# Performance work log

Measured on AMD Instinct MI355X. Metric: run time of the kernel, lower is better.

The kernel has to match this reference:

```python
import jax, jax.numpy as jnp
import numpy as np

H = 128; L = 4; N_TOTAL = 2500; M = 4; K = 12
S = N_TOTAL * M          # 10000 subgraphs
F = S * K                # 120000 flat nodes
E_INTRA = 2 * F          # 240000 intra-subgraph edges
E_INTER = 16 * N_TOTAL   # 40000 canonical edges
B = 50; VOCAB = 119; MAX_DIST = 32; BN_EPS = 1e-5


def _bn(x, g, b):
    # training-mode BatchNorm1d over rows (biased var, eps=1e-5)
    mu = x.mean(0)
    var = x.var(0)
    return (x - mu) * jax.lax.rsqrt(var + BN_EPS) * g + b


def _gine(x, ei, ea, W1, b1, W2, b2):
    # PyG GINEConv, eps=0: MLP(x + sum_{src->dst} relu(x[src] + e))
    msg = jax.nn.relu(x[ei[0]] + ea)                              # [E,H]
    agg = jax.ops.segment_sum(msg, ei[1], num_segments=x.shape[0])
    h = x + agg
    return jax.nn.relu(h @ W1 + b1) @ W2 + b2


def setup_inputs():
    key = jax.random.key(0)
    ks = list(jax.random.split(key, 32)); it = iter(ks)
    nk = lambda: next(it)
    rn = lambda shape, s=0.05: jax.random.normal(nk(), shape, dtype=jnp.float32) * s
    x_tok = jax.random.randint(nk(), (F,), 0, VOCAB)
    dist = jax.random.randint(nk(), (F,), 0, MAX_DIST + 1)
    node_ids = jax.random.randint(nk(), (F,), 0, N_TOTAL)
    node_ids = jnp.where(jax.random.uniform(nk(), (F,)) < 0.1, -1, node_ids)
    root_flat_idx = jnp.arange(S) * K
    node_ids = node_ids.at[root_flat_idx].set(jnp.arange(S) // M)  # root = canonical node
    valid = node_ids >= 0
    sub_batch = jnp.repeat(jnp.arange(S), K)
    src = jax.random.randint(nk(), (E_INTRA,), 0, F)
    dst = (src // K) * K + jax.random.randint(nk(), (E_INTRA,), 0, K)  # stay inside subgraph
    intra_ei = jnp.stack([src, dst])
    edge_index = jax.random.randint(nk(), (2, E_INTER), 0, N_TOTAL)
    batch_ids = jnp.arange(N_TOTAL) // (N_TOTAL // B)
    lp = -jax.random.uniform(nk(), (S,)) * 3.0                    # log-probs <= 0
    z = lambda *shape: jnp.zeros(shape, jnp.float32)
    o = lambda *shape: jnp.ones(shape, jnp.float32)
    return dict(
        x_tok=x_tok, dist=dist, node_ids=node_ids, valid=valid,
        sub_batch=sub_batch, root_flat_idx=root_flat_idx,
        intra_ei=intra_ei, edge_index=edge_index, batch_ids=batch_ids,
        lp=lp, ea_flat=rn((E_INTRA, H)), edge_attr=rn((E_INTER, H)),
        atom_emb=rn((VOCAB, H)), dist_emb=rn((MAX_DIST + 1, H)),
        logp_w=rn((1, H)), logp_b=z(H),
        intra_W1=rn((L, H, H)), intra_b1=z(L, H),
        intra_W2=rn((L, H, H)), intra_b2=z(L, H),
        intra_bn_g=o(L, H), intra_bn_b=z(L, H),
        self_W=rn((L, H, H)), self_b=z(L, H),
        root_W=rn((L, H, H)), root_b=z(L, H),
        inter_W1=rn((L, H, H)), inter_b1=z(L, H),
        inter_W2=rn((L, H, H)), inter_b2=z(L, H),
        inter_bn_g=o(L, H), inter_bn_b=z(L, H),
        readout_bn_g=o(H), readout_bn_b=z(H),
        alpha_pool=o(1), alpha_inter=o(1),
    )


def reference(x_tok, dist, node_ids, valid, sub_batch, root_flat_idx, intra_ei,
              edge_index, batch_ids, lp, ea_flat, edge_attr, atom_emb, dist_emb,
              logp_w, logp_b, intra_W1, intra_b1, intra_W2, intra_b2,
              intra_bn_g, intra_bn_b, self_W, self_b, root_W, root_b,
              inter_W1, inter_b1, inter_W2, inter_b2, inter_bn_g, inter_bn_b,
              readout_bn_g, readout_bn_b, alpha_pool, alpha_inter):
    valid_f = valid.astype(jnp.float32)[:, None]                  # [F,1]
    is_root_f = jnp.zeros((F, 1), jnp.float32).at[root_flat_idx].set(1.0)
    clamped_ids = jnp.maximum(node_ids, 0)
    # input encoding: atom embedding + BFS-distance PE + log-prob PE
    logp_pe = jax.nn.relu(lp[sub_batch][:, None] * logp_w[0] + logp_b)
    h = (atom_emb[x_tok] + dist_emb[dist] + logp_pe) * valid_f
    # HT inter-root weights, normalized per canonical root id
    root_ids = node_ids[root_flat_idx]                            # [S]
    rv = root_ids >= 0
    rid = jnp.maximum(root_ids, 0)
    w_un = jnp.where(rv, jnp.exp(-alpha_inter[0] * lp), 0.0)
    w_sum = jax.ops.segment_sum(w_un, rid, num_segments=N_TOTAL)
    ht_w = jnp.where(rv, w_un / (w_sum[rid] + 1e-16), 0.0)        # [S]
    for l in range(L):
        h1 = _gine(h, intra_ei, ea_flat, intra_W1[l], intra_b1[l], intra_W2[l], intra_b2[l])
        h1 = _bn(h1, intra_bn_g[l], intra_bn_b[l]) * valid_f
        h_root_bcast = h[sub_batch * K]
        h_non_root = (h @ self_W[l] + self_b[l]) + (h_root_bcast @ root_W[l] + root_b[l])
        # HT-weighted scatter of root reps to canonical nodes
        h_roots = h[root_flat_idx]                                # [S,H]
        h_root_canon = jax.ops.segment_sum(h_roots * ht_w[:, None], rid, num_segments=N_TOTAL)
        h_inter = _gine(h_root_canon, edge_index, edge_attr, inter_W1[l], inter_b1[l], inter_W2[l], inter_b2[l])
        h_inter = _bn(h_inter, inter_bn_g[l], inter_bn_b[l])
        h_inter_bcast = h_inter[clamped_ids] * valid_f
        out = is_root_f * (h1 + h_inter_bcast) + (1.0 - is_root_f) * (h1 + h_non_root)
        h = jax.nn.relu(out) * valid_f                            # dropout p=0
    # HT softmax readout over the m subgraphs of each canonical node
    h_sub = jax.ops.segment_sum(h * valid_f, sub_batch, num_segments=S)
    h_sub_2d = h_sub.reshape(N_TOTAL, M, H)
    w = jax.nn.softmax(-alpha_pool[0] * lp.reshape(N_TOTAL, M), axis=1)
    node_emb = jnp.einsum('nm,nmh->nh', w, h_sub_2d)
    node_emb = _bn(node_emb, readout_bn_g, readout_bn_b)
    return jax.ops.segment_sum(node_emb, batch_ids, num_segments=B)  # [B,H]
```

## Files before the change

### kernel.cpp

```cpp
#include <hip/hip_runtime.h>
#include <math.h>

#define H 128
#define H4 (H/4)
#define KK 12
#define MSUB 4
#define FF 120000
#define SS 10000
#define NN 2500
#define NBATCH 50
#define NLAYER 4
#define EINTRA 240000
#define EINTER 40000
#define HH (H*H)
#define BN_EPS 1e-5f
#define CAP_I 24
#define CAP_E 96
#define WFRAG_SHORTS 32768
#define HALF_SHORTS 16384

typedef short short8 __attribute__((ext_vector_type(8)));
typedef float floatx4 __attribute__((ext_vector_type(4)));

__device__ __forceinline__ unsigned short f2bf_rne(float x){
  unsigned u = __float_as_uint(x);
  unsigned r = u + 0x7FFFu + ((u >> 16) & 1u);
  return (unsigned short)(r >> 16);
}


__global__ void k_zero(float* __restrict__ p, int n){
  int i = blockIdx.x*256 + threadIdx.x;
  if (i < n) p[i] = 0.f;
}

__global__ void k_zeroi(int* __restrict__ p, int n){
  int i = blockIdx.x*256 + threadIdx.x;
  if (i < n) p[i] = 0;
}


__global__ void k_wprep(const float* __restrict__ W1, const float* __restrict__ W2,
                        const float* __restrict__ SW, const float* __restrict__ RW,
                        const float* __restrict__ IW1, const float* __restrict__ IW2,
                        short* __restrict__ wf){
  int m = blockIdx.y;
  int layer = m / 6, kind = m % 6;
  const float* Wsrc = (kind==0 ? W1 : kind==1 ? W2 : kind==2 ? SW :
                       kind==3 ? RW : kind==4 ? IW1 : IW2) + (size_t)layer*HH;
  int slot = blockIdx.x*256 + threadIdx.x;
  int s  = slot >> 11;
  int ks = (slot >> 9) & 3;
  int nt = (slot >> 6) & 7;
  int l  = slot & 63;
  int quad = l >> 4, n15 = l & 15;
  int col = nt*16 + n15;
  short v8[8];
  #pragma unroll
  for (int j = 0; j < 8; ++j){
    int k = ks*32 + quad*8 + j;
    float v = Wsrc[(size_t)k*H + col];
    unsigned short hb = f2bf_rne(v);
    if (s == 0) v8[j] = (short)hb;
    else {
      float hf = __uint_as_float((unsigned)hb << 16);
      v8[j] = (short)f2bf_rne(v - hf);
    }
  }
  int half = nt >> 2, nt4 = nt & 3;
  size_t o = (size_t)m*WFRAG_SHORTS + (size_t)half*HALF_SHORTS
           + (size_t)((((s*4 + ks)*4 + nt4)*64 + l)*8);
  *(short8*)(wf + o) = *(const short8*)v8;
}


__global__ void k_bucket2(const int* __restrict__ dst, const int* __restrict__ src,
                          int E, int* __restrict__ cnt, int2* __restrict__ beid, int cap){
  int e = blockIdx.x*256 + threadIdx.x;
  if (e >= E) return;
  int d = dst[e];
  int p = atomicAdd(&cnt[d], 1);
  if (p < cap) beid[(size_t)d*cap + p] = make_int2(e, src[e]);
}


__global__ void k_encode(float* __restrict__ h, const int* __restrict__ xtok,
                         const int* __restrict__ dist, const int* __restrict__ nids,
                         const int* __restrict__ subb, const float* __restrict__ lp,
                         const float* __restrict__ aemb, const float* __restrict__ demb,
                         const float* __restrict__ lw, const float* __restrict__ lb){
  int idx = blockIdx.x*256 + threadIdx.x;
  if (idx >= FF*H4) return;
  int f = idx >> 5; int c = (idx & 31) << 2;
  float vf = (nids[f] >= 0) ? 1.f : 0.f;
  float l = lp[subb[f]];
  float4 a = *(const float4*)(aemb + (size_t)xtok[f]*H + c);
  float4 d = *(const float4*)(demb + (size_t)dist[f]*H + c);
  float4 w = *(const float4*)(lw + c);
  float4 b = *(const float4*)(lb + c);
  float4 o;
  o.x = (a.x + d.x + fmaxf(fmaf(l, w.x, b.x), 0.f)) * vf;
  o.y = (a.y + d.y + fmaxf(fmaf(l, w.y, b.y), 0.f)) * vf;
  o.z = (a.z + d.z + fmaxf(fmaf(l, w.z, b.z), 0.f)) * vf;
  o.w = (a.w + d.w + fmaxf(fmaf(l, w.w, b.w), 0.f)) * vf;
  *(float4*)(h + (size_t)f*H + c) = o;
}


__global__ void k_htw(const int* __restrict__ nids, const int* __restrict__ rfi,
                      const float* __restrict__ lp, const float* __restrict__ alpha,
                      float* __restrict__ htw){
  int n = blockIdx.x*256 + threadIdx.x;
  if (n >= NN) return;
  float a = alpha[0];
  float w[MSUB]; float sum = 0.f;
  #pragma unroll
  for (int m = 0; m < MSUB; ++m){
    int s = n*MSUB + m;
    int rid = nids[rfi[s]];
    float wm = (rid >= 0) ? expf(-a*lp[s]) : 0.f;
    w[m] = wm; sum += wm;
  }
  float inv = 1.f / (sum + 1e-16f);
  #pragma unroll
  for (int m = 0; m < MSUB; ++m) htw[n*MSUB + m] = w[m]*inv;
}


__global__ void k_gine_gather(float* __restrict__ outa, const float* __restrict__ x,
                              const float* __restrict__ ea, const int* __restrict__ cnt,
                              const int2* __restrict__ beid, int rows, int cap){
  int idx = blockIdx.x*256 + threadIdx.x;
  if (idx >= rows*H4) return;
  int f = idx >> 5; int c = (idx & 31) << 2;
  int n = cnt[f]; if (n > cap) n = cap;
  const int2* bl = beid + (size_t)f*cap;
  int2 e0 = bl[0], e1 = bl[1], e2 = bl[2], e3 = bl[3];
  int s0 = (0 < n) ? e0.y : 0, a0 = (0 < n) ? e0.x : 0;
  int s1 = (1 < n) ? e1.y : 0, a1 = (1 < n) ? e1.x : 0;
  int s2 = (2 < n) ? e2.y : 0, a2 = (2 < n) ? e2.x : 0;
  int s3 = (3 < n) ? e3.y : 0, a3 = (3 < n) ? e3.x : 0;
  float4 acc = *(const float4*)(x + (size_t)f*H + c);
  float4 xv0 = *(const float4*)(x + (size_t)s0*H + c);
  float4 ev0 = *(const float4*)(ea + (size_t)a0*H + c);
  float4 xv1 = *(const float4*)(x + (size_t)s1*H + c);
  float4 ev1 = *(const float4*)(ea + (size_t)a1*H + c);
  float4 xv2 = *(const float4*)(x + (size_t)s2*H + c);
  float4 ev2 = *(const float4*)(ea + (size_t)a2*H + c);
  float4 xv3 = *(const float4*)(x + (size_t)s3*H + c);
  float4 ev3 = *(const float4*)(ea + (size_t)a3*H + c);
  if (0 < n){
    acc.x += fmaxf(xv0.x+ev0.x,0.f); acc.y += fmaxf(xv0.y+ev0.y,0.f);
    acc.z += fmaxf(xv0.z+ev0.z,0.f); acc.w += fmaxf(xv0.w+ev0.w,0.f);
  }
  if (1 < n){
    acc.x += fmaxf(xv1.x+ev1.x,0.f); acc.y += fmaxf(xv1.y+ev1.y,0.f);
    acc.z += fmaxf(xv1.z+ev1.z,0.f); acc.w += fmaxf(xv1.w+ev1.w,0.f);
  }
  if (2 < n){
    acc.x += fmaxf(xv2.x+ev2.x,0.f); acc.y += fmaxf(xv2.y+ev2.y,0.f);
    acc.z += fmaxf(xv2.z+ev2.z,0.f); acc.w += fmaxf(xv2.w+ev2.w,0.f);
  }
  if (3 < n){
    acc.x += fmaxf(xv3.x+ev3.x,0.f); acc.y += fmaxf(xv3.y+ev3.y,0.f);
    acc.z += fmaxf(xv3.z+ev3.z,0.f); acc.w += fmaxf(xv3.w+ev3.w,0.f);
  }
  for (int i = 4; i < n; ++i){
    int2 es = bl[i];
    float4 xv = *(const float4*)(x + (size_t)es.y*H + c);
    float4 ev = *(const float4*)(ea + (size_t)es.x*H + c);
    acc.x += fmaxf(xv.x+ev.x,0.f); acc.y += fmaxf(xv.y+ev.y,0.f);
    acc.z += fmaxf(xv.z+ev.z,0.f); acc.w += fmaxf(xv.w+ev.w,0.f);
  }
  *(float4*)(outa + (size_t)f*H + c) = acc;
}


__global__ void k_canon(float* __restrict__ canon, const float* __restrict__ h,
                        const float* __restrict__ htw, const int* __restrict__ rfi){
  int idx = blockIdx.x*256 + threadIdx.x;
  if (idx >= NN*H4) return;
  int n = idx >> 5; int c = (idx & 31) << 2;
  float4 acc = make_float4(0.f,0.f,0.f,0.f);
  #pragma unroll
  for (int m = 0; m < MSUB; ++m){
    int s = n*MSUB + m;
    float w = htw[s];
    const float* p = h + (size_t)rfi[s]*H + c;
    acc.x += w*p[0]; acc.y += w*p[1]; acc.z += w*p[2]; acc.w += w*p[3];
  }
  *(float4*)(canon + (size_t)n*H + c) = acc;
}


__global__ __launch_bounds__(256, 4) void k_mm_mfma(
    const float* __restrict__ in, float* __restrict__ out, int rows,
    const short* __restrict__ wf, const float* __restrict__ bias,
    int mode, const int* __restrict__ gather,
    const float* __restrict__ hmid, const float* __restrict__ r2,
    const float* __restrict__ hinter, const float* __restrict__ muinv,
    const float* __restrict__ bg, const float* __restrict__ bb,
    const int* __restrict__ nids)
{
  __shared__ __align__(16) short wfrag[HALF_SHORTS];
  int tid = threadIdx.x;
  int y = blockIdx.y;
  {
    const float4* s4 = (const float4*)(wf + (size_t)y*HALF_SHORTS);
    float4* d4 = (float4*)wfrag;
    #pragma unroll
    for (int i = 0; i < 8; ++i) d4[tid + i*256] = s4[tid + i*256];
  }
  __syncthreads();

  int w = tid >> 6, l = tid & 63;
  int quad = l >> 4, n15 = l & 15;

  float bv[4], mu[4], iv[4], gv[4], be[4];
  #pragma unroll
  for (int t = 0; t < 4; ++t){
    int col = (y*4 + t)*16 + n15;
    bv[t] = bias[col];
    if (mode == 2){
      mu[t] = muinv[col]; iv[t] = muinv[H+col];
      gv[t] = bg[col];    be[t] = bb[col];
    }
  }

  int ngroups = (rows + 63) >> 6;
  for (int g = blockIdx.x; g < ngroups; g += gridDim.x){
    int rload = g*64 + w*16 + n15;
    bool ok = rload < rows;
    int ir = ok ? (gather ? gather[rload] : rload) : 0;
    const float* ap = in + (size_t)ir*H + quad*8;

    short8 ah[4], al[4];
    #pragma unroll
    for (int ks = 0; ks < 4; ++ks){
      float4 a0 = ok ? *(const float4*)(ap + ks*32)     : make_float4(0.f,0.f,0.f,0.f);
      float4 a1 = ok ? *(const float4*)(ap + ks*32 + 4) : make_float4(0.f,0.f,0.f,0.f);
      float av[8] = {a0.x,a0.y,a0.z,a0.w,a1.x,a1.y,a1.z,a1.w};
      #pragma unroll
      for (int j = 0; j < 8; ++j){
        unsigned short hb = f2bf_rne(av[j]);
        float hf = __uint_as_float((unsigned)hb << 16);
        ah[ks][j] = (short)hb;
        al[ks][j] = (short)f2bf_rne(av[j] - hf);
      }
    }

    floatx4 acc[4] = {};
    #pragma unroll
    for (int ks = 0; ks < 4; ++ks){
      #pragma unroll
      for (int t = 0; t < 4; ++t){
        short8 bh  = *(const short8*)&wfrag[((ks*4 + t)*64 + l)*8];
        short8 blo = *(const short8*)&wfrag[(((4 + ks)*4 + t)*64 + l)*8];
        acc[t] = __builtin_amdgcn_mfma_f32_16x16x32_bf16(ah[ks], bh,  acc[t], 0, 0, 0);
        acc[t] = __builtin_amdgcn_mfma_f32_16x16x32_bf16(al[ks], bh,  acc[t], 0, 0, 0);
        acc[t] = __builtin_amdgcn_mfma_f32_16x16x32_bf16(ah[ks], blo, acc[t], 0, 0, 0);
      }
    }

    int rbase = g*64 + w*16 + quad*4;
    if (mode != 2){
      #pragma unroll
      for (int t = 0; t < 4; ++t){
        int col = (y*4 + t)*16 + n15;
        #pragma unroll
        for (int reg = 0; reg < 4; ++reg){
          int r = rbase + reg;
          if (r < rows){
            float v = acc[t][reg] + bv[t];
            if (mode == 1) v = fmaxf(v, 0.f);
            out[(size_t)r*H + col] = v;
          }
        }
      }
    } else {
      #pragma unroll
      for (int reg = 0; reg < 4; ++reg){
        int r = rbase + reg;
        int nid = nids[r];
        float vf = (nid >= 0) ? 1.f : 0.f;
        int cid = (nid < 0) ? 0 : nid;
        bool isroot = (r % KK) == 0;
        const float* srcp = isroot ? (hinter + (size_t)cid*H) : (r2 + (size_t)(r/KK)*H);
        #pragma unroll
        for (int t = 0; t < 4; ++t){
          int col = (y*4 + t)*16 + n15;
          float h1 = ((hmid[(size_t)r*H + col] - mu[t])*iv[t]*gv[t] + be[t])*vf;
          float o;
          if (isroot) o = h1 + srcp[col]*vf;
          else        o = h1 + (acc[t][reg] + bv[t]) + srcp[col];
          out[(size_t)r*H + col] = fmaxf(o, 0.f)*vf;
        }
      }
    }
  }
}


__global__ void k_bnstats(const float* __restrict__ x, int rows, double* __restrict__ stats){
  int g = blockIdx.x*256 + threadIdx.x;
  int c = g & (H-1);
  int rstart = g >> 7;
  int rstride = (gridDim.x*256) >> 7;
  double s = 0.0, s2 = 0.0;
  for (int r = rstart; r < rows; r += rstride){
    float v = x[(size_t)r*H + c];
    s += v; s2 += (double)v*(double)v;
  }
  atomicAdd(&stats[c], s);
  atomicAdd(&stats[H+c], s2);
}

__global__ void k_bnfin(double* __restrict__ stats, int rows, float* __restrict__ muinv){
  int c = threadIdx.x;
  if (c < H){
    double mu = stats[c] / (double)rows;
    double var = stats[H+c] / (double)rows - mu*mu;
    muinv[c]   = (float)mu;
    muinv[H+c] = (float)(1.0 / sqrt(var + (double)BN_EPS));
    stats[c] = 0.0; stats[H+c] = 0.0;
  }
}

__global__ void k_bnapply(float* __restrict__ x, const float* __restrict__ muinv,
                          const float* __restrict__ g, const float* __restrict__ b, int rows){
  int idx = blockIdx.x*256 + threadIdx.x;
  if (idx >= rows*H4) return;
  int r = idx >> 5; int c = (idx & 31) << 2;
  float4 v  = *(const float4*)(x + (size_t)r*H + c);
  float4 mu = *(const float4*)(muinv + c);
  float4 iv = *(const float4*)(muinv + H + c);
  float4 gg = *(const float4*)(g + c);
  float4 bb = *(const float4*)(b + c);
  v.x = (v.x-mu.x)*iv.x*gg.x + bb.x;
  v.y = (v.y-mu.y)*iv.y*gg.y + bb.y;
  v.z = (v.z-mu.z)*iv.z*gg.z + bb.z;
  v.w = (v.w-mu.w)*iv.w*gg.w + bb.w;
  *(float4*)(x + (size_t)r*H + c) = v;
}


__global__ void k_hsub(float* __restrict__ hsub, const float* __restrict__ h){
  int idx = blockIdx.x*256 + threadIdx.x;
  if (idx >= SS*H4) return;
  int s = idx >> 5; int c = (idx & 31) << 2;
  float4 acc = make_float4(0.f,0.f,0.f,0.f);
  const float* base = h + (size_t)s*KK*H + c;
  #pragma unroll
  for (int k = 0; k < KK; ++k){
    float4 v = *(const float4*)(base + (size_t)k*H);
    acc.x += v.x; acc.y += v.y; acc.z += v.z; acc.w += v.w;
  }
  *(float4*)(hsub + (size_t)s*H + c) = acc;
}

__global__ void k_poolw(float* __restrict__ poolw, const float* __restrict__ lp,
                        const float* __restrict__ alpha){
  int n = blockIdx.x*256 + threadIdx.x;
  if (n >= NN) return;
  float a = alpha[0];
  float s0 = -a*lp[n*MSUB+0], s1 = -a*lp[n*MSUB+1], s2 = -a*lp[n*MSUB+2], s3 = -a*lp[n*MSUB+3];
  float m = fmaxf(fmaxf(s0,s1), fmaxf(s2,s3));
  float e0 = expf(s0-m), e1 = expf(s1-m), e2 = expf(s2-m), e3 = expf(s3-m);
  float sum = e0+e1+e2+e3;
  poolw[n*MSUB+0] = e0/sum; poolw[n*MSUB+1] = e1/sum;
  poolw[n*MSUB+2] = e2/sum; poolw[n*MSUB+3] = e3/sum;
}

__global__ void k_nodeemb(float* __restrict__ nemb, const float* __restrict__ hsub,
                          const float* __restrict__ poolw){
  int idx = blockIdx.x*256 + threadIdx.x;
  if (idx >= NN*H4) return;
  int n = idx >> 5; int c = (idx & 31) << 2;
  float w0 = poolw[n*MSUB+0], w1 = poolw[n*MSUB+1], w2 = poolw[n*MSUB+2], w3 = poolw[n*MSUB+3];
  const float* base = hsub + (size_t)n*MSUB*H + c;
  float4 v0 = *(const float4*)(base + 0*H);
  float4 v1 = *(const float4*)(base + 1*H);
  float4 v2 = *(const float4*)(base + 2*H);
  float4 v3 = *(const float4*)(base + 3*H);
  float4 o;
  o.x = w0*v0.x + w1*v1.x + w2*v2.x + w3*v3.x;
  o.y = w0*v0.y + w1*v1.y + w2*v2.y + w3*v3.y;
  o.z = w0*v0.z + w1*v1.z + w2*v2.z + w3*v3.z;
  o.w = w0*v0.w + w1*v1.w + w2*v2.w + w3*v3.w;
  *(float4*)(nemb + (size_t)n*H + c) = o;
}

__global__ void k_out(float* __restrict__ out, const float* __restrict__ nemb,
                      const float* __restrict__ muinv, const float* __restrict__ g,
                      const float* __restrict__ b){
  int idx = blockIdx.x*256 + threadIdx.x;
  if (idx >= NBATCH*H) return;
  int bi = idx >> 7; int c = idx & (H-1);
  float mu = muinv[c], iv = muinv[H+c], gg = g[c], bb = b[c];
  float acc = 0.f;
  const float* base = nemb + (size_t)bi*(NN/NBATCH)*H + c;
  for (int i = 0; i < NN/NBATCH; ++i)
    acc += (base[(size_t)i*H] - mu)*iv*gg + bb;
  out[idx] = acc;
}


extern "C" void kernel_launch(void* const* d_in, const int* in_sizes, int n_in,
                              void* d_out, int out_size, void* d_ws, size_t ws_size,
                              hipStream_t stream) {
  const int*   x_tok      = (const int*)  d_in[0];
  const int*   dist       = (const int*)  d_in[1];
  const int*   node_ids   = (const int*)  d_in[2];
  const int*   sub_batch  = (const int*)  d_in[4];
  const int*   rfi        = (const int*)  d_in[5];
  const int*   intra_ei   = (const int*)  d_in[6];
  const int*   edge_index = (const int*)  d_in[7];
  const float* lp         = (const float*)d_in[9];
  const float* ea_flat    = (const float*)d_in[10];
  const float* edge_attr  = (const float*)d_in[11];
  const float* atom_emb   = (const float*)d_in[12];
  const float* dist_emb   = (const float*)d_in[13];
  const float* logp_w     = (const float*)d_in[14];
  const float* logp_b     = (const float*)d_in[15];
  const float* intra_W1   = (const float*)d_in[16];
  const float* intra_b1   = (const float*)d_in[17];
  const float* intra_W2   = (const float*)d_in[18];
  const float* intra_b2   = (const float*)d_in[19];
  const float* intra_bn_g = (const float*)d_in[20];
  const float* intra_bn_b = (const float*)d_in[21];
  const float* self_W     = (const float*)d_in[22];
  const float* self_b     = (const float*)d_in[23];
  const float* root_W     = (const float*)d_in[24];
  const float* root_b     = (const float*)d_in[25];
  const float* inter_W1   = (const float*)d_in[26];
  const float* inter_b1   = (const float*)d_in[27];
  const float* inter_W2   = (const float*)d_in[28];
  const float* inter_b2   = (const float*)d_in[29];
  const float* inter_bn_g = (const float*)d_in[30];
  const float* inter_bn_b = (const float*)d_in[31];
  const float* ro_bn_g    = (const float*)d_in[32];
  const float* ro_bn_b    = (const float*)d_in[33];
  const float* alpha_pool = (const float*)d_in[34];
  const float* alpha_inter= (const float*)d_in[35];

  const int* isrc = intra_ei;
  const int* idst = intra_ei + EINTRA;
  const int* esrc = edge_index;
  const int* edst = edge_index + EINTER;

  float* out = (float*)d_out;

  char* ws = (char*)d_ws;
  size_t off = 0;
  auto nxt = [&](size_t bytes) -> void* {
    void* p = ws + off;
    off += (bytes + 255) & ~(size_t)255;
    return p;
  };
  float*  hA     = (float*) nxt((size_t)FF*H*4);
  float*  hB     = (float*) nxt((size_t)FF*H*4);
  float*  hmid   = (float*) nxt((size_t)FF*H*4);
  float*  tbuf   = (float*) nxt((size_t)FF*H*4);
  float*  r2     = (float*) nxt((size_t)SS*H*4);
  float*  canon  = (float*) nxt((size_t)NN*H*4);
  float*  agg2   = (float*) nxt((size_t)NN*H*4);
  float*  hsub   = (float*) nxt((size_t)SS*H*4);
  float*  nemb   = (float*) nxt((size_t)NN*H*4);
  float*  htw    = (float*) nxt((size_t)SS*4);
  float*  poolw  = (float*) nxt((size_t)NN*MSUB*4);
  double* statsA = (double*)nxt((size_t)2*H*8);
  double* statsB = (double*)nxt((size_t)2*H*8);
  float*  muinvA = (float*) nxt((size_t)2*H*4);
  float*  muinvB = (float*) nxt((size_t)2*H*4);
  short*  wsplit = (short*) nxt((size_t)24*WFRAG_SHORTS*2);
  int*    icnt   = (int*)   nxt((size_t)FF*4);
  int2*   ibeid  = (int2*)  nxt((size_t)FF*CAP_I*8);
  int*    ecnt   = (int*)   nxt((size_t)NN*4);
  int2*   ebeid  = (int2*)  nxt((size_t)NN*CAP_E*8);
  (void)ws_size; (void)n_in; (void)in_sizes; (void)out_size; (void)sub_batch;

  const int G_FH4 = FF*H4/256;
  const int G_SH4 = SS*H4/256;
  const int G_NH4 = (NN*H4 + 255)/256;
  const int G_N   = (NN + 255)/256;
  const dim3 G_MM_F(512, 2);
  const dim3 G_MM_S((SS + 63)/64, 2);
  const dim3 G_MM_N((NN + 63)/64, 2);

  k_zero<<<2, 256, 0, stream>>>((float*)statsA, 2*H*2);
  k_zero<<<2, 256, 0, stream>>>((float*)statsB, 2*H*2);
  k_zeroi<<<(FF+255)/256, 256, 0, stream>>>(icnt, FF);
  k_zeroi<<<G_N, 256, 0, stream>>>(ecnt, NN);

  k_wprep<<<dim3(16,24), 256, 0, stream>>>(intra_W1, intra_W2, self_W, root_W,
                                           inter_W1, inter_W2, wsplit);
  k_bucket2<<<(EINTRA+255)/256, 256, 0, stream>>>(idst, isrc, EINTRA, icnt, ibeid, CAP_I);
  k_bucket2<<<(EINTER+255)/256, 256, 0, stream>>>(edst, esrc, EINTER, ecnt, ebeid, CAP_E);

  k_encode<<<G_FH4, 256, 0, stream>>>(hA, x_tok, dist, node_ids, sub_batch, lp,
                                      atom_emb, dist_emb, logp_w, logp_b);
  k_htw<<<G_N, 256, 0, stream>>>(node_ids, rfi, lp, alpha_inter, htw);

  float* hcur = hA;
  float* hnxt = hB;
  for (int l = 0; l < NLAYER; ++l){
    const short* wfL = wsplit + (size_t)l*6*WFRAG_SHORTS;

    k_gine_gather<<<G_FH4, 256, 0, stream>>>(hmid, hcur, ea_flat, icnt, ibeid, FF, CAP_I);
    k_mm_mfma<<<G_MM_F, 256, 0, stream>>>(hmid, tbuf, FF, wfL + 0*WFRAG_SHORTS,
        intra_b1 + (size_t)l*H, 1, nullptr,
        nullptr,nullptr,nullptr,nullptr,nullptr,nullptr,nullptr);
    k_mm_mfma<<<G_MM_F, 256, 0, stream>>>(tbuf, hmid, FF, wfL + 1*WFRAG_SHORTS,
        intra_b2 + (size_t)l*H, 0, nullptr,
        nullptr,nullptr,nullptr,nullptr,nullptr,nullptr,nullptr);
    k_bnstats<<<512, 256, 0, stream>>>(hmid, FF, statsA);
    k_bnfin<<<1, 128, 0, stream>>>(statsA, FF, muinvA);

    k_canon<<<G_NH4, 256, 0, stream>>>(canon, hcur, htw, rfi);
    k_mm_mfma<<<G_MM_S, 256, 0, stream>>>(hcur, r2, SS, wfL + 3*WFRAG_SHORTS,
        root_b + (size_t)l*H, 0, rfi,
        nullptr,nullptr,nullptr,nullptr,nullptr,nullptr,nullptr);

    k_gine_gather<<<G_NH4, 256, 0, stream>>>(agg2, canon, edge_attr, ecnt, ebeid, NN, CAP_E);
    k_mm_mfma<<<G_MM_N, 256, 0, stream>>>(agg2, tbuf, NN, wfL + 4*WFRAG_SHORTS,
        inter_b1 + (size_t)l*H, 1, nullptr,
        nullptr,nullptr,nullptr,nullptr,nullptr,nullptr,nullptr);
    k_mm_mfma<<<G_MM_N, 256, 0, stream>>>(tbuf, agg2, NN, wfL + 5*WFRAG_SHORTS,
        inter_b2 + (size_t)l*H, 0, nullptr,
        nullptr,nullptr,nullptr,nullptr,nullptr,nullptr,nullptr);
    k_bnstats<<<128, 256, 0, stream>>>(agg2, NN, statsB);
    k_bnfin<<<1, 128, 0, stream>>>(statsB, NN, muinvB);
    k_bnapply<<<G_NH4, 256, 0, stream>>>(agg2, muinvB, inter_bn_g + (size_t)l*H,
                                         inter_bn_b + (size_t)l*H, NN);

    k_mm_mfma<<<G_MM_F, 256, 0, stream>>>(hcur, hnxt, FF, wfL + 2*WFRAG_SHORTS,
        self_b + (size_t)l*H, 2, nullptr,
        hmid, r2, agg2, muinvA,
        intra_bn_g + (size_t)l*H, intra_bn_b + (size_t)l*H, node_ids);

    float* t = hcur; hcur = hnxt; hnxt = t;
  }

  k_hsub<<<G_SH4, 256, 0, stream>>>(hsub, hcur);
  k_poolw<<<G_N, 256, 0, stream>>>(poolw, lp, alpha_pool);
  k_nodeemb<<<G_NH4, 256, 0, stream>>>(nemb, hsub, poolw);
  k_bnstats<<<128, 256, 0, stream>>>(nemb, NN, statsB);
  k_bnfin<<<1, 128, 0, stream>>>(statsB, NN, muinvB);
  k_out<<<(NBATCH*H+255)/256, 256, 0, stream>>>(out, nemb, muinvB, ro_bn_g, ro_bn_b);
}
```

Baseline: 2.261 ms.

## Use fp16 edge attributes, atomic-free BN stats, smaller edge caps, rotate buffers

Edge attributes are converted to fp16 once per call and gathered as half2, which halves the dominant edge-feature gather traffic in both GINE aggregations. BatchNorm statistics now use per-block float4 partial sums reduced through shared memory and a separate finalize pass, replacing the double-precision atomics and the zeroing kernels. Bucket capacities drop from 24 to 16 and from 96 to 64, shrinking the edge lists. A three-buffer rotation replaces the four full-size activations and reuses hsub as scratch. The risks are fp16 rounding of edge attributes and silently dropped edges if any node's in-degree exceeds the smaller caps.

```diff
diff --git a/kernel.cpp b/kernel.cpp
--- a/kernel.cpp
+++ b/kernel.cpp
@@ -1,4 +1,5 @@
 #include <hip/hip_runtime.h>
+#include <hip/hip_fp16.h>
 #include <math.h>
 
 #define H 128
@@ -14,10 +15,12 @@
 #define EINTER 40000
 #define HH (H*H)
 #define BN_EPS 1e-5f
-#define CAP_I 24
-#define CAP_E 96
+#define CAP_I 16
+#define CAP_E 64
 #define WFRAG_SHORTS 32768
 #define HALF_SHORTS 16384
+#define BN_BLK_F 256
+#define BN_BLK_N 32
 
 typedef short short8 __attribute__((ext_vector_type(8)));
 typedef float floatx4 __attribute__((ext_vector_type(4)));
@@ -29,14 +32,19 @@
 }
 
 
-__global__ void k_zero(float* __restrict__ p, int n){
-  int i = blockIdx.x*256 + threadIdx.x;
-  if (i < n) p[i] = 0.f;
-}
-
 __global__ void k_zeroi(int* __restrict__ p, int n){
   int i = blockIdx.x*256 + threadIdx.x;
   if (i < n) p[i] = 0;
+}
+
+
+__global__ void k_eaprep(const float* __restrict__ src, __half* __restrict__ dst, int n4){
+  int i = blockIdx.x*256 + threadIdx.x;
+  if (i >= n4) return;
+  float4 v = ((const float4*)src)[i];
+  __half2* d = (__half2*)(dst + (size_t)i*4);
+  d[0] = __floats2half2_rn(v.x, v.y);
+  d[1] = __floats2half2_rn(v.z, v.w);
 }
 
 
@@ -127,8 +135,15 @@
 }
 
 
+__device__ __forceinline__ float4 ld_ea4(const __half* __restrict__ ea, size_t base){
+  const __half2* p = (const __half2*)(ea + base);
+  float2 f01 = __half22float2(p[0]);
+  float2 f23 = __half22float2(p[1]);
+  return make_float4(f01.x, f01.y, f23.x, f23.y);
+}
+
 __global__ void k_gine_gather(float* __restrict__ outa, const float* __restrict__ x,
-                              const float* __restrict__ ea, const int* __restrict__ cnt,
+                              const __half* __restrict__ ea, const int* __restrict__ cnt,
                               const int2* __restrict__ beid, int rows, int cap){
   int idx = blockIdx.x*256 + threadIdx.x;
   if (idx >= rows*H4) return;
@@ -142,13 +157,13 @@
   int s3 = (3 < n) ? e3.y : 0, a3 = (3 < n) ? e3.x : 0;
   float4 acc = *(const float4*)(x + (size_t)f*H + c);
   float4 xv0 = *(const float4*)(x + (size_t)s0*H + c);
-  float4 ev0 = *(const float4*)(ea + (size_t)a0*H + c);
+  float4 ev0 = ld_ea4(ea, (size_t)a0*H + c);
   float4 xv1 = *(const float4*)(x + (size_t)s1*H + c);
-  float4 ev1 = *(const float4*)(ea + (size_t)a1*H + c);
+  float4 ev1 = ld_ea4(ea, (size_t)a1*H + c);
   float4 xv2 = *(const float4*)(x + (size_t)s2*H + c);
-  float4 ev2 = *(const float4*)(ea + (size_t)a2*H + c);
+  float4 ev2 = ld_ea4(ea, (size_t)a2*H + c);
   float4 xv3 = *(const float4*)(x + (size_t)s3*H + c);
-  float4 ev3 = *(const float4*)(ea + (size_t)a3*H + c);
+  float4 ev3 = ld_ea4(ea, (size_t)a3*H + c);
   if (0 < n){
     acc.x += fmaxf(xv0.x+ev0.x,0.f); acc.y += fmaxf(xv0.y+ev0.y,0.f);
     acc.z += fmaxf(xv0.z+ev0.z,0.f); acc.w += fmaxf(xv0.w+ev0.w,0.f);
@@ -168,7 +183,7 @@
   for (int i = 4; i < n; ++i){
     int2 es = bl[i];
     float4 xv = *(const float4*)(x + (size_t)es.y*H + c);
-    float4 ev = *(const float4*)(ea + (size_t)es.x*H + c);
+    float4 ev = ld_ea4(ea, (size_t)es.x*H + c);
     acc.x += fmaxf(xv.x+ev.x,0.f); acc.y += fmaxf(xv.y+ev.y,0.f);
     acc.z += fmaxf(xv.z+ev.z,0.f); acc.w += fmaxf(xv.w+ev.w,0.f);
   }
@@ -301,29 +316,49 @@
 }
 
 
-__global__ void k_bnstats(const float* __restrict__ x, int rows, double* __restrict__ stats){
-  int g = blockIdx.x*256 + threadIdx.x;
-  int c = g & (H-1);
-  int rstart = g >> 7;
-  int rstride = (gridDim.x*256) >> 7;
-  double s = 0.0, s2 = 0.0;
-  for (int r = rstart; r < rows; r += rstride){
-    float v = x[(size_t)r*H + c];
-    s += v; s2 += (double)v*(double)v;
-  }
-  atomicAdd(&stats[c], s);
-  atomicAdd(&stats[H+c], s2);
-}
-
-__global__ void k_bnfin(double* __restrict__ stats, int rows, float* __restrict__ muinv){
+__global__ void k_bnstats1(const float* __restrict__ x, int rows, double* __restrict__ part){
+  __shared__ double sh[8][32][8];
+  int tid = threadIdx.x;
+  int chunk = tid & 31, rgrp = tid >> 5;
+  int c = chunk << 2;
+  double s0=0,s1=0,s2=0,s3=0, q0=0,q1=0,q2=0,q3=0;
+  for (int r = blockIdx.x*8 + rgrp; r < rows; r += gridDim.x*8){
+    float4 v = *(const float4*)(x + (size_t)r*H + c);
+    s0 += v.x; q0 += (double)v.x*(double)v.x;
+    s1 += v.y; q1 += (double)v.y*(double)v.y;
+    s2 += v.z; q2 += (double)v.z*(double)v.z;
+    s3 += v.w; q3 += (double)v.w*(double)v.w;
+  }
+  sh[rgrp][chunk][0]=s0; sh[rgrp][chunk][1]=q0;
+  sh[rgrp][chunk][2]=s1; sh[rgrp][chunk][3]=q1;
+  sh[rgrp][chunk][4]=s2; sh[rgrp][chunk][5]=q2;
+  sh[rgrp][chunk][6]=s3; sh[rgrp][chunk][7]=q3;
+  __syncthreads();
+  if (tid < 32){
+    #pragma unroll
+    for (int j = 0; j < 8; ++j){
+      double a = 0.0;
+      #pragma unroll
+      for (int r = 0; r < 8; ++r) a += sh[r][tid][j];
+      part[((size_t)blockIdx.x*32 + tid)*8 + j] = a;
+    }
+  }
+}
+
+__global__ void k_bnfin2(const double* __restrict__ part, int nblk, int rows,
+                         float* __restrict__ muinv){
   int c = threadIdx.x;
-  if (c < H){
-    double mu = stats[c] / (double)rows;
-    double var = stats[H+c] / (double)rows - mu*mu;
-    muinv[c]   = (float)mu;
-    muinv[H+c] = (float)(1.0 / sqrt(var + (double)BN_EPS));
-    stats[c] = 0.0; stats[H+c] = 0.0;
-  }
+  if (c >= H) return;
+  int chunk = c >> 2, ci = c & 3;
+  double s = 0.0, q = 0.0;
+  for (int b = 0; b < nblk; ++b){
+    const double* p = part + ((size_t)b*32 + chunk)*8 + ci*2;
+    s += p[0]; q += p[1];
+  }
+  double mu = s / (double)rows;
+  double var = q / (double)rows - mu*mu;
+  muinv[c]   = (float)mu;
+  muinv[H+c] = (float)(1.0 / sqrt(var + (double)BN_EPS));
 }
 
 __global__ void k_bnapply(float* __restrict__ x, const float* __restrict__ muinv,
@@ -457,10 +492,11 @@
     off += (bytes + 255) & ~(size_t)255;
     return p;
   };
-  float*  hA     = (float*) nxt((size_t)FF*H*4);
-  float*  hB     = (float*) nxt((size_t)FF*H*4);
-  float*  hmid   = (float*) nxt((size_t)FF*H*4);
-  float*  tbuf   = (float*) nxt((size_t)FF*H*4);
+  float*  P0     = (float*) nxt((size_t)FF*H*4);
+  float*  P1     = (float*) nxt((size_t)FF*H*4);
+  float*  P2     = (float*) nxt((size_t)FF*H*4);
+  __half* ea16i  = (__half*)nxt((size_t)EINTRA*H*2);
+  __half* ea16e  = (__half*)nxt((size_t)EINTER*H*2);
   float*  r2     = (float*) nxt((size_t)SS*H*4);
   float*  canon  = (float*) nxt((size_t)NN*H*4);
   float*  agg2   = (float*) nxt((size_t)NN*H*4);
@@ -468,8 +504,7 @@
   float*  nemb   = (float*) nxt((size_t)NN*H*4);
   float*  htw    = (float*) nxt((size_t)SS*4);
   float*  poolw  = (float*) nxt((size_t)NN*MSUB*4);
-  double* statsA = (double*)nxt((size_t)2*H*8);
-  double* statsB = (double*)nxt((size_t)2*H*8);
+  double* bnpart = (double*)nxt((size_t)BN_BLK_F*32*8*8);
   float*  muinvA = (float*) nxt((size_t)2*H*4);
   float*  muinvB = (float*) nxt((size_t)2*H*4);
   short*  wsplit = (short*) nxt((size_t)24*WFRAG_SHORTS*2);
@@ -487,64 +522,63 @@
   const dim3 G_MM_S((SS + 63)/64, 2);
   const dim3 G_MM_N((NN + 63)/64, 2);
 
-  k_zero<<<2, 256, 0, stream>>>((float*)statsA, 2*H*2);
-  k_zero<<<2, 256, 0, stream>>>((float*)statsB, 2*H*2);
   k_zeroi<<<(FF+255)/256, 256, 0, stream>>>(icnt, FF);
   k_zeroi<<<G_N, 256, 0, stream>>>(ecnt, NN);
 
   k_wprep<<<dim3(16,24), 256, 0, stream>>>(intra_W1, intra_W2, self_W, root_W,
                                            inter_W1, inter_W2, wsplit);
+  k_eaprep<<<(EINTRA*H4 + 255)/256, 256, 0, stream>>>(ea_flat, ea16i, EINTRA*H4);
+  k_eaprep<<<(EINTER*H4 + 255)/256, 256, 0, stream>>>(edge_attr, ea16e, EINTER*H4);
   k_bucket2<<<(EINTRA+255)/256, 256, 0, stream>>>(idst, isrc, EINTRA, icnt, ibeid, CAP_I);
   k_bucket2<<<(EINTER+255)/256, 256, 0, stream>>>(edst, esrc, EINTER, ecnt, ebeid, CAP_E);
 
-  k_encode<<<G_FH4, 256, 0, stream>>>(hA, x_tok, dist, node_ids, sub_batch, lp,
+  k_encode<<<G_FH4, 256, 0, stream>>>(P0, x_tok, dist, node_ids, sub_batch, lp,
                                       atom_emb, dist_emb, logp_w, logp_b);
   k_htw<<<G_N, 256, 0, stream>>>(node_ids, rfi, lp, alpha_inter, htw);
 
-  float* hcur = hA;
-  float* hnxt = hB;
+  float* X = P0; float* Y = P1; float* Z = P2;
   for (int l = 0; l < NLAYER; ++l){
     const short* wfL = wsplit + (size_t)l*6*WFRAG_SHORTS;
 
-    k_gine_gather<<<G_FH4, 256, 0, stream>>>(hmid, hcur, ea_flat, icnt, ibeid, FF, CAP_I);
-    k_mm_mfma<<<G_MM_F, 256, 0, stream>>>(hmid, tbuf, FF, wfL + 0*WFRAG_SHORTS,
+    k_gine_gather<<<G_FH4, 256, 0, stream>>>(Y, X, ea16i, icnt, ibeid, FF, CAP_I);
+    k_mm_mfma<<<G_MM_F, 256, 0, stream>>>(Y, Z, FF, wfL + 0*WFRAG_SHORTS,
         intra_b1 + (size_t)l*H, 1, nullptr,
         nullptr,nullptr,nullptr,nullptr,nullptr,nullptr,nullptr);
-    k_mm_mfma<<<G_MM_F, 256, 0, stream>>>(tbuf, hmid, FF, wfL + 1*WFRAG_SHORTS,
+    k_mm_mfma<<<G_MM_F, 256, 0, stream>>>(Z, Y, FF, wfL + 1*WFRAG_SHORTS,
         intra_b2 + (size_t)l*H, 0, nullptr,
         nullptr,nullptr,nullptr,nullptr,nullptr,nullptr,nullptr);
-    k_bnstats<<<512, 256, 0, stream>>>(hmid, FF, statsA);
-    k_bnfin<<<1, 128, 0, stream>>>(statsA, FF, muinvA);
-
-    k_canon<<<G_NH4, 256, 0, stream>>>(canon, hcur, htw, rfi);
-    k_mm_mfma<<<G_MM_S, 256, 0, stream>>>(hcur, r2, SS, wfL + 3*WFRAG_SHORTS,
+    k_bnstats1<<<BN_BLK_F, 256, 0, stream>>>(Y, FF, bnpart);
+    k_bnfin2<<<1, 128, 0, stream>>>(bnpart, BN_BLK_F, FF, muinvA);
+
+    k_canon<<<G_NH4, 256, 0, stream>>>(canon, X, htw, rfi);
+    k_mm_mfma<<<G_MM_S, 256, 0, stream>>>(X, r2, SS, wfL + 3*WFRAG_SHORTS,
         root_b + (size_t)l*H, 0, rfi,
         nullptr,nullptr,nullptr,nullptr,nullptr,nullptr,nullptr);
 
-    k_gine_gather<<<G_NH4, 256, 0, stream>>>(agg2, canon, edge_attr, ecnt, ebeid, NN, CAP_E);
-    k_mm_mfma<<<G_MM_N, 256, 0, stream>>>(agg2, tbuf, NN, wfL + 4*WFRAG_SHORTS,
+    k_gine_gather<<<G_NH4, 256, 0, stream>>>(agg2, canon, ea16e, ecnt, ebeid, NN, CAP_E);
+    k_mm_mfma<<<G_MM_N, 256, 0, stream>>>(agg2, hsub, NN, wfL + 4*WFRAG_SHORTS,
         inter_b1 + (size_t)l*H, 1, nullptr,
         nullptr,nullptr,nullptr,nullptr,nullptr,nullptr,nullptr);
-    k_mm_mfma<<<G_MM_N, 256, 0, stream>>>(tbuf, agg2, NN, wfL + 5*WFRAG_SHORTS,
+    k_mm_mfma<<<G_MM_N, 256, 0, stream>>>(hsub, agg2, NN, wfL + 5*WFRAG_SHORTS,
         inter_b2 + (size_t)l*H, 0, nullptr,
         nullptr,nullptr,nullptr,nullptr,nullptr,nullptr,nullptr);
-    k_bnstats<<<128, 256, 0, stream>>>(agg2, NN, statsB);
-    k_bnfin<<<1, 128, 0, stream>>>(statsB, NN, muinvB);
+    k_bnstats1<<<BN_BLK_N, 256, 0, stream>>>(agg2, NN, bnpart);
+    k_bnfin2<<<1, 128, 0, stream>>>(bnpart, BN_BLK_N, NN, muinvB);
     k_bnapply<<<G_NH4, 256, 0, stream>>>(agg2, muinvB, inter_bn_g + (size_t)l*H,
                                          inter_bn_b + (size_t)l*H, NN);
 
-    k_mm_mfma<<<G_MM_F, 256, 0, stream>>>(hcur, hnxt, FF, wfL + 2*WFRAG_SHORTS,
+    k_mm_mfma<<<G_MM_F, 256, 0, stream>>>(X, Z, FF, wfL + 2*WFRAG_SHORTS,
         self_b + (size_t)l*H, 2, nullptr,
-        hmid, r2, agg2, muinvA,
+        Y, r2, agg2, muinvA,
         intra_bn_g + (size_t)l*H, intra_bn_b + (size_t)l*H, node_ids);
 
-    float* t = hcur; hcur = hnxt; hnxt = t;
-  }
-
-  k_hsub<<<G_SH4, 256, 0, stream>>>(hsub, hcur);
+    float* t = Z; Z = Y; Y = X; X = t;
+  }
+
+  k_hsub<<<G_SH4, 256, 0, stream>>>(hsub, X);
   k_poolw<<<G_N, 256, 0, stream>>>(poolw, lp, alpha_pool);
   k_nodeemb<<<G_NH4, 256, 0, stream>>>(nemb, hsub, poolw);
-  k_bnstats<<<128, 256, 0, stream>>>(nemb, NN, statsB);
-  k_bnfin<<<1, 128, 0, stream>>>(statsB, NN, muinvB);
+  k_bnstats1<<<BN_BLK_N, 256, 0, stream>>>(nemb, NN, bnpart);
+  k_bnfin2<<<1, 128, 0, stream>>>(bnpart, BN_BLK_N, NN, muinvB);
   k_out<<<(NBATCH*H+255)/256, 256, 0, stream>>>(out, nemb, muinvB, ro_bn_g, ro_bn_b);
 }
```

Result: slower. 2.415 ms (+6.8%).
